# Performance work log

Hardware: AMD Instinct MI355X
Metric: run time of the kernel (lower is better)

## Reference

```python
import jax, jax.numpy as jnp
import numpy as np
import math

N_HEAD = 16
N_HEAD_KV = 4
HEAD_DIM = 128
N_EMBD = 2048

def alibi_slopes(n_heads):
    def pow2_slopes(n):
        start = 2 ** (-2 ** (-(math.log2(n) - 3)))
        return [start * start ** i for i in range(n)]
    if math.log2(n_heads).is_integer():
        return jnp.array(pow2_slopes(n_heads), dtype=jnp.float32)
    closest = 2 ** math.floor(math.log2(n_heads))
    base = pow2_slopes(closest)
    if n_heads <= 2 * closest:
        s = base + base[0::2]
    else:
        s = base + base[0::2] + base[1::2]
    return jnp.array(s[:n_heads], dtype=jnp.float32)

def setup_inputs() -> dict:
    key = jax.random.key(0)
    ks = jax.random.split(key, 5)
    B, T, C = 2, 2048, N_EMBD
    kvdim = N_HEAD_KV * HEAD_DIM
    sc = 0.02
    return {
        "x": jax.random.normal(ks[0], (B, T, C), dtype=jnp.float32),
        "q_w": jax.random.normal(ks[1], (C, C), dtype=jnp.float32) * sc,
        "k_w": jax.random.normal(ks[2], (kvdim, C), dtype=jnp.float32) * sc,
        "v_w": jax.random.normal(ks[3], (kvdim, C), dtype=jnp.float32) * sc,
        "o_w": jax.random.normal(ks[4], (C, C), dtype=jnp.float32) * sc,
    }

def reference(x, q_w, k_w, v_w, o_w):
    B, T, C = x.shape
    H, Hkv, D = N_HEAD, N_HEAD_KV, HEAD_DIM
    # nan/inf sanitize (no-op for random inputs, kept for fidelity)
    x = jnp.nan_to_num(x, nan=0.0, posinf=10000.0, neginf=-10000.0)
    q = (x @ q_w.T).reshape(B, T, H, D).transpose(0, 2, 1, 3)      # [B,H,T,D]
    k = (x @ k_w.T).reshape(B, T, Hkv, D).transpose(0, 2, 1, 3)    # [B,Hkv,T,D]
    v = (x @ v_w.T).reshape(B, T, Hkv, D).transpose(0, 2, 1, 3)
    # repeat_interleave KV heads to H heads
    rep = H // Hkv
    k = jnp.repeat(k, rep, axis=1)
    v = jnp.repeat(v, rep, axis=1)
    scale = 1.0 / math.sqrt(D)
    att = jnp.einsum('bhqd,bhkd->bhqk', q, k) * scale
    att = jnp.clip(att, -10000.0, 10000.0)
    pos = jnp.arange(T)
    causal = jnp.where(pos[None, :] > pos[:, None], -jnp.inf, 0.0)  # [T,T]
    slopes = alibi_slopes(H)  # [H]
    rel = (pos[None, :] - pos[:, None]).astype(jnp.float32)         # [T,T]
    alibi = slopes[:, None, None] * rel[None]                        # [H,T,T]
    att = att + causal[None, None] + alibi[None]
    att = jax.nn.softmax(att.astype(jnp.float32), axis=-1).astype(q.dtype)
    y = jnp.einsum('bhqk,bhkd->bhqd', att, v)
    y = jnp.nan_to_num(y, nan=0.0, posinf=10000.0, neginf=-10000.0)
    y = y.transpose(0, 2, 1, 3).reshape(B, T, C)
    return y @ o_w.T
```

## Files before the change

kernel.cpp:

```cpp
#include <hip/hip_runtime.h>
#include <hip/hip_bf16.h>
#include <math.h>

#define SEQ   2048
#define EMBD  2048
#define NH    16
#define NKV   4
#define HD    128
#define NQKV  3072

typedef __attribute__((ext_vector_type(8))) short short8;
typedef __attribute__((ext_vector_type(4))) short short4v;
typedef __attribute__((ext_vector_type(4))) float floatx4;

static __device__ __forceinline__ short f2bf(float f) {
    union { float f; unsigned u; } cv; cv.f = f;
    unsigned u = cv.u;
    u += 0x7FFF + ((u >> 16) & 1);
    return (short)(u >> 16);
}

#define GL16(gsrc, ldst)                                                        \
    __builtin_amdgcn_global_load_lds(                                           \
        (const __attribute__((address_space(1))) void*)(gsrc),                  \
        (__attribute__((address_space(3))) void*)(ldst), 16, 0, 0)

__global__ void cvt_all(const float* __restrict__ x,  const float* __restrict__ qw,
                        const float* __restrict__ kw, const float* __restrict__ vw,
                        const float* __restrict__ ow,
                        short* __restrict__ xb, short* __restrict__ wall,
                        short* __restrict__ owb) {
    int i = blockIdx.x * blockDim.x + threadIdx.x;
    const float* src; short* dst; int off;
    if (i < 2097152)      { src = x;  dst = xb;             off = i; }
    else if (i < 3145728) { src = qw; dst = wall;           off = i - 2097152; }
    else if (i < 3407872) { src = kw; dst = wall + 4194304; off = i - 3145728; }
    else if (i < 3670016) { src = vw; dst = wall + 5242880; off = i - 3407872; }
    else                  { src = ow; dst = owb;            off = i - 3670016; }
    float4 v = ((const float4*)src)[off];
    float a[4] = {v.x, v.y, v.z, v.w};
    short4v o;
#pragma unroll
    for (int j = 0; j < 4; ++j) {
        float f = a[j];
        f = isnan(f) ? 0.0f : fminf(fmaxf(f, -10000.0f), 10000.0f);
        o[j] = f2bf(f);
    }
    ((short4v*)dst)[off] = o;
}

template<int MODE>
__global__ __launch_bounds__(256) void gemm_bt(
    const short* __restrict__ A, const short* __restrict__ W,
    float* __restrict__ Cout, int M, int N, int K,
    short* __restrict__ qb, short* __restrict__ kb, short* __restrict__ vb)
{
    __shared__ __align__(16) short sA[128 * 32];
    __shared__ __align__(16) short sB[128 * 32];

    const int tid  = threadIdx.x;
    const int lane = tid & 63;
    const int wv   = tid >> 6;
    const int wr   = wv >> 1, wc = wv & 1;
    const int lr   = lane & 15, lg = lane >> 4;
    const int bn   = blockIdx.x, bm = blockIdx.y;

    const short* gA[2]; const short* gB[2];
    short* lA[2]; short* lB[2];
#pragma unroll
    for (int s = 0; s < 2; ++s) {
        int chunk = wv * 128 + s * 64 + lane;
        int row = chunk >> 2, seg = chunk & 3;
        gA[s] = A + (size_t)(bm * 128 + row) * K + seg * 8;
        gB[s] = W + (size_t)(bn * 128 + row) * K + seg * 8;
        lA[s] = &sA[(wv * 128 + s * 64) * 8];
        lB[s] = &sB[(wv * 128 + s * 64) * 8];
    }

    floatx4 acc[4][4] = {};
    const int nkt = K / 32;
    for (int kt = 0; kt < nkt; ++kt) {
#pragma unroll
        for (int s = 0; s < 2; ++s) {
            GL16(gA[s] + kt * 32, lA[s]);
            GL16(gB[s] + kt * 32, lB[s]);
        }
        __syncthreads();

        short8 af[4], bfr[4];
#pragma unroll
        for (int i = 0; i < 4; ++i) {
            af[i]  = *(const short8*)&sA[(wr * 64 + i * 16 + lr) * 32 + lg * 8];
            bfr[i] = *(const short8*)&sB[(wc * 64 + i * 16 + lr) * 32 + lg * 8];
        }
#pragma unroll
        for (int i = 0; i < 4; ++i)
#pragma unroll
            for (int j = 0; j < 4; ++j)
                acc[i][j] = __builtin_amdgcn_mfma_f32_16x16x32_bf16(af[i], bfr[j], acc[i][j], 0, 0, 0);
        __syncthreads();
    }

    const float QSCALE = 0.08838834764831845f * 1.44269504f;
#pragma unroll
    for (int i = 0; i < 4; ++i)
#pragma unroll
        for (int j = 0; j < 4; ++j)
#pragma unroll
            for (int r = 0; r < 4; ++r) {
                int gm = bm * 128 + wr * 64 + i * 16 + lg * 4 + r;
                int gn = bn * 128 + wc * 64 + j * 16 + lr;
                float v = acc[i][j][r];
                if (MODE == 0) {
                    int b = gm >> 11, t = gm & (SEQ - 1);
                    if (gn < 2048) {
                        int h = gn >> 7, d = gn & 127;
                        qb[(((size_t)(b * NH + h)) * SEQ + t) * HD + d] = f2bf(v * QSCALE);
                    } else if (gn < 2560) {
                        int hk = (gn - 2048) >> 7, d = gn & 127;
                        kb[(((size_t)(b * NKV + hk)) * SEQ + t) * HD + d] = f2bf(v);
                    } else {
                        int hv = (gn - 2560) >> 7, d = gn & 127;
                        vb[(((size_t)(b * NKV + hv)) * HD + d) * SEQ + t] = f2bf(v);
                    }
                } else {
                    Cout[(size_t)gm * N + gn] = v;
                }
            }
}

__global__ __launch_bounds__(256) void attn_fwd(
    const short* __restrict__ Q, const short* __restrict__ Kg,
    const short* __restrict__ VT, short* __restrict__ Y)
{
    __shared__ __align__(16) short sK[2][64 * 128];
    __shared__ __align__(16) short sV[2][128 * 64];
    __shared__ short Plds[4][16][72];

    const int tid  = threadIdx.x;
    const int wave = tid >> 6, lane = tid & 63;
    const int lr = lane & 15, lg = lane >> 4;
    const int bid = blockIdx.x;
    const int pid = bid >> 5;
    const int bh  = bid & 31;
    const int b = bh >> 4, h = bh & 15;
    const int hkv = h >> 2;

    const short* Qb = Q  +  ((size_t)(b * NH  + h  )) * SEQ * HD;
    const short* Kp = Kg +  ((size_t)(b * NKV + hkv)) * SEQ * HD;
    const short* Vp = VT +  ((size_t)(b * NKV + hkv)) * HD * SEQ;

    const float slope2 = exp2f(-0.5f * (float)(h + 1)) * 1.44269504f;
    const int W = (int)ceilf((42.0f / slope2 + 63.0f) * (1.0f / 64.0f));

    const short* gK[4]; const short* gV[4];
    int lOff[4];
#pragma unroll
    for (int j = 0; j < 4; ++j) {
        int ck = wave * 256 + j * 64 + lane;
        int krow = ck >> 4, kseg = ck & 15;
        gK[j] = Kp + (size_t)krow * HD + (kseg ^ (krow & 7)) * 8;
        int vrow = ck >> 3, vseg = ck & 7;
        gV[j] = Vp + (size_t)vrow * SEQ + (vseg ^ (vrow & 7)) * 8;
        lOff[j] = (wave * 256 + j * 64) * 8;
    }

    float c_nt[4];
#pragma unroll
    for (int nt = 0; nt < 4; ++nt) c_nt[nt] = slope2 * (float)(nt * 16 + lr);

    int cur = 0;
#pragma unroll 1
    for (int s = 0; s < 2; ++s) {
        const int qg = s == 0 ? (31 - pid) : pid;
        const int q0 = qg * 64 + wave * 16;
        int tmin = qg + 1 - W; if (tmin < 0) tmin = 0;

        short8 qf[4];
#pragma unroll
        for (int c = 0; c < 4; ++c)
            qf[c] = *(const short8*)&Qb[(size_t)(q0 + lr) * HD + c * 32 + lg * 8];

        floatx4 po[8] = {};
        float m[4], lsum[4];
#pragma unroll
        for (int r = 0; r < 4; ++r) { m[r] = -3.0e38f; lsum[r] = 0.0f; }

        {
            const int kv0 = qg << 6;
#pragma unroll
            for (int j = 0; j < 4; ++j) {
                GL16(gK[j] + (size_t)kv0 * HD, &sK[cur][0] + lOff[j]);
                GL16(gV[j] + kv0, &sV[cur][0] + lOff[j]);
            }
        }
        __syncthreads();

#pragma unroll 1
        for (int t = qg; t >= tmin; --t) {
            if (t > tmin) {
                const int kvn = (t - 1) << 6;
#pragma unroll
                for (int j = 0; j < 4; ++j) {
                    GL16(gK[j] + (size_t)kvn * HD, &sK[cur ^ 1][0] + lOff[j]);
                    GL16(gV[j] + kvn, &sV[cur ^ 1][0] + lOff[j]);
                }
            }
            const int kv0 = t << 6;
            const short* kr = &sK[cur][0];
            const short* vr = &sV[cur][0];

            floatx4 sf[4];
#pragma unroll
            for (int nt = 0; nt < 4; ++nt) {
                floatx4 sacc = {0.f, 0.f, 0.f, 0.f};
#pragma unroll
                for (int cc = 0; cc < 4; ++cc) {
                    int krow = nt * 16 + lr;
                    short8 kf = *(const short8*)&kr[krow * 128 + (((cc * 4 + lg) ^ (krow & 7)) * 8)];
                    sacc = __builtin_amdgcn_mfma_f32_16x16x32_bf16(qf[cc], kf, sacc, 0, 0, 0);
                }
                sf[nt] = sacc;
            }

            const float a2t = slope2 * (float)kv0;
            float base[4];
#pragma unroll
            for (int nt = 0; nt < 4; ++nt) base[nt] = a2t + c_nt[nt];
            const bool masked = (t == qg);
#pragma unroll
            for (int r = 0; r < 4; ++r) {
                const int qpos = q0 + lg * 4 + r;
                float sv[4];
#pragma unroll
                for (int nt = 0; nt < 4; ++nt)
                    sv[nt] = sf[nt][r] + base[nt];
                if (masked) {
#pragma unroll
                    for (int nt = 0; nt < 4; ++nt) {
                        int kpos = kv0 + nt * 16 + lr;
                        if (kpos > qpos) sv[nt] = -3.0e38f;
                    }
                }
                bool over = (sv[0] > m[r]) | (sv[1] > m[r]) | (sv[2] > m[r]) | (sv[3] > m[r]);
                if (__any(over)) {
                    float mx = fmaxf(fmaxf(sv[0], sv[1]), fmaxf(sv[2], sv[3]));
#pragma unroll
                    for (int off = 1; off < 16; off <<= 1) mx = fmaxf(mx, __shfl_xor(mx, off));
                    float mn = fmaxf(m[r], mx);
                    float rs = exp2f(m[r] - mn);
                    lsum[r] *= rs;
#pragma unroll
                    for (int dt = 0; dt < 8; ++dt) po[dt][r] *= rs;
                    m[r] = mn;
                }
#pragma unroll
                for (int nt = 0; nt < 4; ++nt) {
                    float p = exp2f(sv[nt] - m[r]);
                    lsum[r] += p;
                    Plds[wave][lg * 4 + r][nt * 16 + lr] = f2bf(p);
                }
            }

            short8 pf0 = *(const short8*)&Plds[wave][lr][lg * 8];
            short8 pf1 = *(const short8*)&Plds[wave][lr][32 + lg * 8];
#pragma unroll
            for (int dt = 0; dt < 8; ++dt) {
                int vrow = dt * 16 + lr;
                short8 vf0 = *(const short8*)&vr[vrow * 64 + (((lg    ) ^ (vrow & 7)) * 8)];
                short8 vf1 = *(const short8*)&vr[vrow * 64 + (((lg + 4) ^ (vrow & 7)) * 8)];
                po[dt] = __builtin_amdgcn_mfma_f32_16x16x32_bf16(pf0, vf0, po[dt], 0, 0, 0);
                po[dt] = __builtin_amdgcn_mfma_f32_16x16x32_bf16(pf1, vf1, po[dt], 0, 0, 0);
            }
            __syncthreads();
            cur ^= 1;
        }

#pragma unroll
        for (int r = 0; r < 4; ++r) {
            float sum = lsum[r];
#pragma unroll
            for (int off = 1; off < 16; off <<= 1) sum += __shfl_xor(sum, off);
            float inv = 1.0f / sum;
            int row = q0 + lg * 4 + r;
#pragma unroll
            for (int dt = 0; dt < 8; ++dt)
                Y[((size_t)(b * SEQ + row)) * EMBD + h * HD + dt * 16 + lr] = f2bf(po[dt][r] * inv);
        }
    }
}

extern "C" void kernel_launch(void* const* d_in, const int* in_sizes, int n_in,
                              void* d_out, int out_size, void* d_ws, size_t ws_size,
                              hipStream_t stream) {
    const float* x   = (const float*)d_in[0];
    const float* q_w = (const float*)d_in[1];
    const float* k_w = (const float*)d_in[2];
    const float* v_w = (const float*)d_in[3];
    const float* o_w = (const float*)d_in[4];
    float* out = (float*)d_out;

    char* ws = (char*)d_ws;
    short* x_bf  = (short*)(ws);
    short* w_all = (short*)(ws + 16777216);
    short* o_wb  = (short*)(ws + 29360128);
    short* q_b   = (short*)(ws + 37748736);
    short* k_b   = (short*)(ws + 54525952);
    short* vT_b  = (short*)(ws + 58720256);
    short* y_b   = (short*)(ws + 62914560);

    cvt_all<<<18432, 256, 0, stream>>>(x, q_w, k_w, v_w, o_w, x_bf, w_all, o_wb);

    gemm_bt<0><<<dim3(NQKV / 128, 4096 / 128), 256, 0, stream>>>(
        x_bf, w_all, nullptr, 4096, NQKV, EMBD, q_b, k_b, vT_b);

    attn_fwd<<<512, 256, 0, stream>>>(q_b, k_b, vT_b, y_b);

    gemm_bt<1><<<dim3(EMBD / 128, 4096 / 128), 256, 0, stream>>>(
        y_b, o_wb, out, 4096, EMBD, EMBD, nullptr, nullptr, nullptr);
}
```

Before: 240.9 us.

## Split long ALiBi-window heads across two blocks and merge partials

The attention grid changes from paired query-tile blocks to one block per query tile. The six heads with the widest ALiBi window (h>=10) have their KV range split across two blocks, and each writes unnormalized partial outputs plus max and sum to workspace. A new combine kernel merges the two partials with log-sum-exp rescaling. This aims to balance load and raise parallelism for the long-window heads, at the cost of an extra launch and fp32 partial traffic. The partial buffer reuses the workspace region that held x_bf, which is dead after the QKV GEMM.

New measurement: 265.4 us. 1.1x slower.

```diff
diff --git a/kernel.cpp b/kernel.cpp
--- a/kernel.cpp
+++ b/kernel.cpp
@@ -8,6 +8,8 @@
 #define NKV   4
 #define HD    128
 #define NQKV  3072
+#define NHEAVY 6
+#define HVY0  10
 
 typedef __attribute__((ext_vector_type(8))) short short8;
 typedef __attribute__((ext_vector_type(4))) short short4v;
@@ -24,6 +26,10 @@
     __builtin_amdgcn_global_load_lds(                                           \
         (const __attribute__((address_space(1))) void*)(gsrc),                  \
         (__attribute__((address_space(3))) void*)(ldst), 16, 0, 0)
+
+static __device__ __forceinline__ int alibi_window(float slope2) {
+    return (int)ceilf((42.0f / slope2 + 63.0f) * (1.0f / 64.0f));
+}
 
 __global__ void cvt_all(const float* __restrict__ x,  const float* __restrict__ qw,
                         const float* __restrict__ kw, const float* __restrict__ vw,
@@ -131,7 +137,8 @@
 
 __global__ __launch_bounds__(256) void attn_fwd(
     const short* __restrict__ Q, const short* __restrict__ Kg,
-    const short* __restrict__ VT, short* __restrict__ Y)
+    const short* __restrict__ VT, short* __restrict__ Y,
+    float* __restrict__ part)
 {
     __shared__ __align__(16) short sK[2][64 * 128];
     __shared__ __align__(16) short sV[2][128 * 64];
@@ -141,17 +148,33 @@
     const int wave = tid >> 6, lane = tid & 63;
     const int lr = lane & 15, lg = lane >> 4;
     const int bid = blockIdx.x;
-    const int pid = bid >> 5;
-    const int bh  = bid & 31;
-    const int b = bh >> 4, h = bh & 15;
+
+    int b, h, qg, c; bool heavy;
+    if (bid < 768) {
+        heavy = true;
+        c = bid & 1; qg = (bid >> 1) & 31;
+        int hb = bid >> 6; int hh = hb % NHEAVY; b = hb / NHEAVY; h = HVY0 + hh;
+    } else {
+        heavy = false; c = 0;
+        int u = bid - 768;
+        qg = u & 31;
+        int hb = u >> 5; h = hb % HVY0; b = hb / HVY0;
+    }
     const int hkv = h >> 2;
+
+    const float slope2 = exp2f(-0.5f * (float)(h + 1)) * 1.44269504f;
+    const int W = alibi_window(slope2);
+    const int L = min(W, qg + 1);
+    const int blo = qg + 1 - L;
+    int thi, tlo;
+    if (heavy) {
+        if (c == 0) { thi = qg; tlo = max(blo, qg - 15); }
+        else        { thi = qg - 16; tlo = blo; if (thi < tlo) return; }
+    } else { thi = qg; tlo = blo; }
 
     const short* Qb = Q  +  ((size_t)(b * NH  + h  )) * SEQ * HD;
     const short* Kp = Kg +  ((size_t)(b * NKV + hkv)) * SEQ * HD;
     const short* Vp = VT +  ((size_t)(b * NKV + hkv)) * HD * SEQ;
-
-    const float slope2 = exp2f(-0.5f * (float)(h + 1)) * 1.44269504f;
-    const int W = (int)ceilf((42.0f / slope2 + 63.0f) * (1.0f / 64.0f));
 
     const short* gK[4]; const short* gV[4];
     int lOff[4];
@@ -169,113 +192,109 @@
 #pragma unroll
     for (int nt = 0; nt < 4; ++nt) c_nt[nt] = slope2 * (float)(nt * 16 + lr);
 
+    const int q0 = qg * 64 + wave * 16;
+    short8 qf[4];
+#pragma unroll
+    for (int cc = 0; cc < 4; ++cc)
+        qf[cc] = *(const short8*)&Qb[(size_t)(q0 + lr) * HD + cc * 32 + lg * 8];
+
+    floatx4 po[8] = {};
+    float m[4], lsum[4];
+#pragma unroll
+    for (int r = 0; r < 4; ++r) { m[r] = -3.0e38f; lsum[r] = 0.0f; }
+
     int cur = 0;
+    {
+        const int kv0 = thi << 6;
+#pragma unroll
+        for (int j = 0; j < 4; ++j) {
+            GL16(gK[j] + (size_t)kv0 * HD, &sK[cur][0] + lOff[j]);
+            GL16(gV[j] + kv0, &sV[cur][0] + lOff[j]);
+        }
+    }
+    __syncthreads();
+
 #pragma unroll 1
-    for (int s = 0; s < 2; ++s) {
-        const int qg = s == 0 ? (31 - pid) : pid;
-        const int q0 = qg * 64 + wave * 16;
-        int tmin = qg + 1 - W; if (tmin < 0) tmin = 0;
-
-        short8 qf[4];
-#pragma unroll
-        for (int c = 0; c < 4; ++c)
-            qf[c] = *(const short8*)&Qb[(size_t)(q0 + lr) * HD + c * 32 + lg * 8];
-
-        floatx4 po[8] = {};
-        float m[4], lsum[4];
-#pragma unroll
-        for (int r = 0; r < 4; ++r) { m[r] = -3.0e38f; lsum[r] = 0.0f; }
-
-        {
-            const int kv0 = qg << 6;
+    for (int t = thi; t >= tlo; --t) {
+        if (t > tlo) {
+            const int kvn = (t - 1) << 6;
 #pragma unroll
             for (int j = 0; j < 4; ++j) {
-                GL16(gK[j] + (size_t)kv0 * HD, &sK[cur][0] + lOff[j]);
-                GL16(gV[j] + kv0, &sV[cur][0] + lOff[j]);
-            }
+                GL16(gK[j] + (size_t)kvn * HD, &sK[cur ^ 1][0] + lOff[j]);
+                GL16(gV[j] + kvn, &sV[cur ^ 1][0] + lOff[j]);
+            }
+        }
+        const int kv0 = t << 6;
+        const short* kr = &sK[cur][0];
+        const short* vr = &sV[cur][0];
+
+        floatx4 sf[4];
+#pragma unroll
+        for (int nt = 0; nt < 4; ++nt) {
+            floatx4 sacc = {0.f, 0.f, 0.f, 0.f};
+#pragma unroll
+            for (int cc = 0; cc < 4; ++cc) {
+                int krow = nt * 16 + lr;
+                short8 kf = *(const short8*)&kr[krow * 128 + (((cc * 4 + lg) ^ (krow & 7)) * 8)];
+                sacc = __builtin_amdgcn_mfma_f32_16x16x32_bf16(qf[cc], kf, sacc, 0, 0, 0);
+            }
+            sf[nt] = sacc;
+        }
+
+        const float a2t = slope2 * (float)kv0;
+        float base[4];
+#pragma unroll
+        for (int nt = 0; nt < 4; ++nt) base[nt] = a2t + c_nt[nt];
+        const bool masked = (t == qg);
+#pragma unroll
+        for (int r = 0; r < 4; ++r) {
+            const int qpos = q0 + lg * 4 + r;
+            float sv[4];
+#pragma unroll
+            for (int nt = 0; nt < 4; ++nt)
+                sv[nt] = sf[nt][r] + base[nt];
+            if (masked) {
+#pragma unroll
+                for (int nt = 0; nt < 4; ++nt) {
+                    int kpos = kv0 + nt * 16 + lr;
+                    if (kpos > qpos) sv[nt] = -3.0e38f;
+                }
+            }
+            bool over = (sv[0] > m[r]) | (sv[1] > m[r]) | (sv[2] > m[r]) | (sv[3] > m[r]);
+            if (__any(over)) {
+                float mx = fmaxf(fmaxf(sv[0], sv[1]), fmaxf(sv[2], sv[3]));
+#pragma unroll
+                for (int off = 1; off < 16; off <<= 1) mx = fmaxf(mx, __shfl_xor(mx, off));
+                float mn = fmaxf(m[r], mx);
+                float rs = exp2f(m[r] - mn);
+                lsum[r] *= rs;
+#pragma unroll
+                for (int dt = 0; dt < 8; ++dt) po[dt][r] *= rs;
+                m[r] = mn;
+            }
+#pragma unroll
+            for (int nt = 0; nt < 4; ++nt) {
+                float p = exp2f(sv[nt] - m[r]);
+                lsum[r] += p;
+                Plds[wave][lg * 4 + r][nt * 16 + lr] = f2bf(p);
+            }
+        }
+
+        short8 pf0 = *(const short8*)&Plds[wave][lr][lg * 8];
+        short8 pf1 = *(const short8*)&Plds[wave][lr][32 + lg * 8];
+#pragma unroll
+        for (int dt = 0; dt < 8; ++dt) {
+            int vrow = dt * 16 + lr;
+            short8 vf0 = *(const short8*)&vr[vrow * 64 + (((lg    ) ^ (vrow & 7)) * 8)];
+            short8 vf1 = *(const short8*)&vr[vrow * 64 + (((lg + 4) ^ (vrow & 7)) * 8)];
+            po[dt] = __builtin_amdgcn_mfma_f32_16x16x32_bf16(pf0, vf0, po[dt], 0, 0, 0);
+            po[dt] = __builtin_amdgcn_mfma_f32_16x16x32_bf16(pf1, vf1, po[dt], 0, 0, 0);
         }
         __syncthreads();
-
-#pragma unroll 1
-        for (int t = qg; t >= tmin; --t) {
-            if (t > tmin) {
-                const int kvn = (t - 1) << 6;
-#pragma unroll
-                for (int j = 0; j < 4; ++j) {
-                    GL16(gK[j] + (size_t)kvn * HD, &sK[cur ^ 1][0] + lOff[j]);
-                    GL16(gV[j] + kvn, &sV[cur ^ 1][0] + lOff[j]);
-                }
-            }
-            const int kv0 = t << 6;
-            const short* kr = &sK[cur][0];
-            const short* vr = &sV[cur][0];
-
-            floatx4 sf[4];
-#pragma unroll
-            for (int nt = 0; nt < 4; ++nt) {
-                floatx4 sacc = {0.f, 0.f, 0.f, 0.f};
-#pragma unroll
-                for (int cc = 0; cc < 4; ++cc) {
-                    int krow = nt * 16 + lr;
-                    short8 kf = *(const short8*)&kr[krow * 128 + (((cc * 4 + lg) ^ (krow & 7)) * 8)];
-                    sacc = __builtin_amdgcn_mfma_f32_16x16x32_bf16(qf[cc], kf, sacc, 0, 0, 0);
-                }
-                sf[nt] = sacc;
-            }
-
-            const float a2t = slope2 * (float)kv0;
-            float base[4];
-#pragma unroll
-            for (int nt = 0; nt < 4; ++nt) base[nt] = a2t + c_nt[nt];
-            const bool masked = (t == qg);
-#pragma unroll
-            for (int r = 0; r < 4; ++r) {
-                const int qpos = q0 + lg * 4 + r;
-                float sv[4];
-#pragma unroll
-                for (int nt = 0; nt < 4; ++nt)
-                    sv[nt] = sf[nt][r] + base[nt];
-                if (masked) {
-#pragma unroll
-                    for (int nt = 0; nt < 4; ++nt) {
-                        int kpos = kv0 + nt * 16 + lr;
-                        if (kpos > qpos) sv[nt] = -3.0e38f;
-                    }
-                }
-                bool over = (sv[0] > m[r]) | (sv[1] > m[r]) | (sv[2] > m[r]) | (sv[3] > m[r]);
-                if (__any(over)) {
-                    float mx = fmaxf(fmaxf(sv[0], sv[1]), fmaxf(sv[2], sv[3]));
-#pragma unroll
-                    for (int off = 1; off < 16; off <<= 1) mx = fmaxf(mx, __shfl_xor(mx, off));
-                    float mn = fmaxf(m[r], mx);
-                    float rs = exp2f(m[r] - mn);
-                    lsum[r] *= rs;
-#pragma unroll
-                    for (int dt = 0; dt < 8; ++dt) po[dt][r] *= rs;
-                    m[r] = mn;
-                }
-#pragma unroll
-                for (int nt = 0; nt < 4; ++nt) {
-                    float p = exp2f(sv[nt] - m[r]);
-                    lsum[r] += p;
-                    Plds[wave][lg * 4 + r][nt * 16 + lr] = f2bf(p);
-                }
-            }
-
-            short8 pf0 = *(const short8*)&Plds[wave][lr][lg * 8];
-            short8 pf1 = *(const short8*)&Plds[wave][lr][32 + lg * 8];
-#pragma unroll
-            for (int dt = 0; dt < 8; ++dt) {
-                int vrow = dt * 16 + lr;
-                short8 vf0 = *(const short8*)&vr[vrow * 64 + (((lg    ) ^ (vrow & 7)) * 8)];
-                short8 vf1 = *(const short8*)&vr[vrow * 64 + (((lg + 4) ^ (vrow & 7)) * 8)];
-                po[dt] = __builtin_amdgcn_mfma_f32_16x16x32_bf16(pf0, vf0, po[dt], 0, 0, 0);
-                po[dt] = __builtin_amdgcn_mfma_f32_16x16x32_bf16(pf1, vf1, po[dt], 0, 0, 0);
-            }
-            __syncthreads();
-            cur ^= 1;
-        }
-
+        cur ^= 1;
+    }
+
+    if (!heavy) {
 #pragma unroll
         for (int r = 0; r < 4; ++r) {
             float sum = lsum[r];
@@ -287,7 +306,50 @@
             for (int dt = 0; dt < 8; ++dt)
                 Y[((size_t)(b * SEQ + row)) * EMBD + h * HD + dt * 16 + lr] = f2bf(po[dt][r] * inv);
         }
-    }
+    } else {
+        int pu = ((b * NHEAVY + (h - HVY0)) * 32 + qg) * 2 + c;
+        float* pw = part + (size_t)pu * 64 * 130;
+#pragma unroll
+        for (int r = 0; r < 4; ++r) {
+            float sum = lsum[r];
+#pragma unroll
+            for (int off = 1; off < 16; off <<= 1) sum += __shfl_xor(sum, off);
+            int rr = wave * 16 + lg * 4 + r;
+#pragma unroll
+            for (int dt = 0; dt < 8; ++dt)
+                pw[rr * 130 + dt * 16 + lr] = po[dt][r];
+            if (lr == 0) { pw[rr * 130 + 128] = m[r]; pw[rr * 130 + 129] = sum; }
+        }
+    }
+}
+
+__global__ void attn_combine(const float* __restrict__ part, short* __restrict__ Y) {
+    const int tid = threadIdx.x;
+    const int rg  = blockIdx.x * 2 + (tid >> 7);
+    const int col = tid & 127;
+    const int b = rg / (NHEAVY * SEQ);
+    const int rem = rg % (NHEAVY * SEQ);
+    const int hh = rem >> 11, trow = rem & (SEQ - 1);
+    const int h = HVY0 + hh;
+    const int qg = trow >> 6, rr = trow & 63;
+
+    const float slope2 = exp2f(-0.5f * (float)(h + 1)) * 1.44269504f;
+    const int W = alibi_window(slope2);
+    const int L = min(W, qg + 1);
+
+    const float* p0 = part + ((size_t)(((b * NHEAVY + hh) * 32 + qg) * 2) * 64 + rr) * 130;
+    float v;
+    float m0 = p0[128], l0 = p0[129];
+    if (L > 16) {
+        const float* p1 = p0 + 64 * 130;
+        float m1 = p1[128], l1 = p1[129];
+        float M = fmaxf(m0, m1);
+        float s0 = exp2f(m0 - M), s1 = exp2f(m1 - M);
+        v = (p0[col] * s0 + p1[col] * s1) / (l0 * s0 + l1 * s1);
+    } else {
+        v = p0[col] / l0;
+    }
+    Y[((size_t)(b * SEQ + trow)) * EMBD + h * HD + col] = f2bf(v);
 }
 
 extern "C" void kernel_launch(void* const* d_in, const int* in_sizes, int n_in,
@@ -308,13 +370,15 @@
     short* k_b   = (short*)(ws + 54525952);
     short* vT_b  = (short*)(ws + 58720256);
     short* y_b   = (short*)(ws + 62914560);
+    float* part  = (float*)(ws);
 
     cvt_all<<<18432, 256, 0, stream>>>(x, q_w, k_w, v_w, o_w, x_bf, w_all, o_wb);
 
     gemm_bt<0><<<dim3(NQKV / 128, 4096 / 128), 256, 0, stream>>>(
         x_bf, w_all, nullptr, 4096, NQKV, EMBD, q_b, k_b, vT_b);
 
-    attn_fwd<<<512, 256, 0, stream>>>(q_b, k_b, vT_b, y_b);
+    attn_fwd<<<768 + 640, 256, 0, stream>>>(q_b, k_b, vT_b, y_b, part);
+    attn_combine<<<NHEAVY * SEQ, 256, 0, stream>>>(part, y_b);
 
     gemm_bt<1><<<dim3(EMBD / 128, 4096 / 128), 256, 0, stream>>>(
         y_b, o_wb, out, 4096, EMBD, EMBD, nullptr, nullptr, nullptr);
```
